# Kernel tuning notes

Hardware: AMD Instinct MI355X
Metric: run time of the kernel (lower is better)

## Reference

```python
import jax, jax.numpy as jnp
import numpy as np
from jax.scipy.special import logsumexp

EPS = 0.05        # entropic regularization (blur^p)
N_ITERS = 20      # Sinkhorn iterations
N, M, D = 8192, 8192, 64


def setup_inputs() -> dict:
    key = jax.random.key(0)
    k1, k2, k3, k4 = jax.random.split(key, 4)
    return {
        "a": jax.random.uniform(k1, (N,), dtype=jnp.float32),
        "x": jax.random.normal(k2, (N, D), dtype=jnp.float32),
        "b": jax.random.uniform(k3, (M,), dtype=jnp.float32),
        "y": jax.random.normal(k4, (M, D), dtype=jnp.float32),
    }


def reference(a, x, b, y):
    eps = EPS
    # _normalize_weights: probability simplex
    a = a / jnp.sum(a)
    b = b / jnp.sum(b)
    loga = jnp.log(a)
    logb = jnp.log(b)
    # squared-Euclidean cost C_ij = ||x_i - y_j||^2, built via one GEMM (online kernel's math)
    x2 = jnp.sum(x * x, axis=1)            # [N]
    y2 = jnp.sum(y * y, axis=1)            # [M]
    C = x2[:, None] + y2[None, :] - 2.0 * (x @ y.T)   # [N, M]

    # log-domain Sinkhorn: f_i = -eps * LSE_j( log b_j + (g_j - C_ij)/eps )
    def softmin_rows(g_, C_, logw):   # reduce over columns j -> [N]
        return -eps * logsumexp(logw[None, :] + (g_[None, :] - C_) / eps, axis=1)

    def softmin_cols(f_, C_, logw):   # reduce over rows i -> [M]
        return -eps * logsumexp(logw[:, None] + (f_[:, None] - C_) / eps, axis=0)

    def body(i, fg):
        f_, g_ = fg
        f_ = softmin_rows(g_, C, logb)
        g_ = softmin_cols(f_, C, loga)
        return (f_, g_)

    f0 = jnp.zeros_like(a)
    g0 = jnp.zeros_like(b)
    f, g = jax.lax.fori_loop(0, N_ITERS, body, (f0, g0))

    # GeomLoss-style: one final symmetric update from detached potentials (Danskin)
    f_d = jax.lax.stop_gradient(f)
    g_d = jax.lax.stop_gradient(g)
    f_fin = softmin_rows(g_d, C, logb)
    g_fin = softmin_cols(f_d, C, loga)
    # OT_eps(a, b) = <a, f> + <b, g>
    return jnp.sum(a * f_fin) + jnp.sum(b * g_fin)
```

## Files before the change

### kernel.cpp

```cpp
#include <hip/hip_runtime.h>
#include <hip/hip_bf16.h>

#define EPS       0.05f
#define N_ITERS   20
#define NR        8192
#define DIM       64
#define LOG2E     1.4426950408889634f
#define LN2       0.6931471805599453f
#define S2        (2.0f * LOG2E / EPS)
#define EPSLN2    (EPS * LN2)
#define NEGINF    (-1e30f)
#define NSPLIT    4

typedef __attribute__((ext_vector_type(8))) short short8;
typedef __attribute__((ext_vector_type(4))) float float4v;

__device__ __forceinline__ float wave_reduce_sum(float v) {
    #pragma unroll
    for (int m = 1; m < 64; m <<= 1) v += __shfl_xor(v, m, 64);
    return v;
}

__device__ __forceinline__ float merge4_l(float2 p0, float2 p1, float2 p2, float2 p3) {
    float M = fmaxf(fmaxf(p0.x, p1.x), fmaxf(p2.x, p3.x));
    float S = p0.y * __builtin_amdgcn_exp2f(p0.x - M)
            + p1.y * __builtin_amdgcn_exp2f(p1.x - M)
            + p2.y * __builtin_amdgcn_exp2f(p2.x - M)
            + p3.y * __builtin_amdgcn_exp2f(p3.x - M);
    return M + __builtin_amdgcn_logf(S);
}

__global__ void sums_kernel(const float* __restrict__ a, const float* __restrict__ b,
                            float* __restrict__ sums) {
    __shared__ float red[32];
    int tid = threadIdx.x;
    float pa = 0.f, pb = 0.f;
    for (int i = tid; i < NR; i += blockDim.x) { pa += a[i]; pb += b[i]; }
    pa = wave_reduce_sum(pa);
    pb = wave_reduce_sum(pb);
    int wid = tid >> 6, ln = tid & 63;
    if (ln == 0) { red[wid] = pa; red[wid + 16] = pb; }
    __syncthreads();
    if (tid == 0) {
        float sa = 0.f, sb = 0.f;
        int nw = blockDim.x >> 6;
        for (int w = 0; w < nw; w++) { sa += red[w]; sb += red[w + 16]; }
        sums[0] = logf(sa); sums[1] = logf(sb); sums[2] = sa; sums[3] = sb;
    }
}

__global__ void prep_kernel(const float* __restrict__ x, const float* __restrict__ y,
                            const float* __restrict__ a, const float* __restrict__ b,
                            const float* __restrict__ sums,
                            short8* __restrict__ xr, short8* __restrict__ yr,
                            short8* __restrict__ xs, short8* __restrict__ ys,
                            float* __restrict__ x2, float* __restrict__ y2,
                            float* __restrict__ la2, float* __restrict__ lb2,
                            float2* __restrict__ Pb) {
    int gid = blockIdx.x * 256 + threadIdx.x;
    bool isx = gid < NR * 8;
    int cid = isx ? gid : gid - NR * 8;
    int row = cid >> 3;
    int c   = cid & 7;
    const float4* src = (const float4*)(isx ? x : y);
    float4 v0 = src[row * 16 + c * 2];
    float4 v1 = src[row * 16 + c * 2 + 1];

    short8 st;
    st[0] = __bfloat16_as_short(__float2bfloat16(v0.x));
    st[1] = __bfloat16_as_short(__float2bfloat16(v0.y));
    st[2] = __bfloat16_as_short(__float2bfloat16(v0.z));
    st[3] = __bfloat16_as_short(__float2bfloat16(v0.w));
    st[4] = __bfloat16_as_short(__float2bfloat16(v1.x));
    st[5] = __bfloat16_as_short(__float2bfloat16(v1.y));
    st[6] = __bfloat16_as_short(__float2bfloat16(v1.z));
    st[7] = __bfloat16_as_short(__float2bfloat16(v1.w));

    (isx ? xr : yr)[row * 8 + c] = st;
    int T = row >> 4, ln = row & 15, f = c >> 2, q = c & 3;
    (isx ? xs : ys)[T * 128 + f * 64 + q * 16 + ln] = st;

    float sq = v0.x*v0.x + v0.y*v0.y + v0.z*v0.z + v0.w*v0.w
             + v1.x*v1.x + v1.y*v1.y + v1.z*v1.z + v1.w*v1.w;
    #pragma unroll
    for (int m = 1; m < 8; m <<= 1) sq += __shfl_xor(sq, m, 64);

    if (c == 0) {
        if (isx) {
            x2[row] = sq;
            la2[row] = (logf(a[row]) - sums[0]) * LOG2E;
        } else {
            y2[row] = sq;
            lb2[row] = (logf(b[row]) - sums[1]) * LOG2E;
            Pb[row] = make_float2(sq * (LOG2E / EPS), 1.0f);
            #pragma unroll
            for (int k = 1; k < NSPLIT; k++)
                Pb[k * NR + row] = make_float2(NEGINF, 0.0f);
        }
    }
}

#define LSE4(acc, c4, mm, ss)                                            \
    {                                                                    \
        float z0 = fmaf(S2, (acc)[0], (c4).x);                           \
        float z1 = fmaf(S2, (acc)[1], (c4).y);                           \
        float z2 = fmaf(S2, (acc)[2], (c4).z);                           \
        float z3 = fmaf(S2, (acc)[3], (c4).w);                           \
        float zm = fmaxf(fmaxf(z0, z1), fmaxf(z2, z3));                  \
        float mn = fmaxf((mm), zm);                                      \
        float e  = __builtin_amdgcn_exp2f((mm) - mn);                    \
        float p  = (__builtin_amdgcn_exp2f(z0 - mn)                      \
                  + __builtin_amdgcn_exp2f(z1 - mn))                     \
                 + (__builtin_amdgcn_exp2f(z2 - mn)                      \
                  + __builtin_amdgcn_exp2f(z3 - mn));                    \
        (ss) = fmaf((ss), e, p);                                         \
        (mm) = mn;                                                       \
    }

__global__ __launch_bounds__(1024, 4) void pass_kernel(
        const short8* __restrict__ matXr,
        const short8* __restrict__ matYs,
        const float2* __restrict__ Pin,
        const float* __restrict__ lw2col,
        float2* __restrict__ Pout) {
    __shared__ __attribute__((aligned(16))) float cbl[2048];
    __shared__ float2 comb[128][9];

    const int tid = threadIdx.x;
    const int bi  = blockIdx.x;
    const int q4  = bi & 3;
    const int rb  = (bi >> 2) * 128;
    const int cb0 = q4 * 2048;

    {
        int j = cb0 + tid * 2;
        float4 p0 = *(const float4*)(Pin + 0 * NR + j);
        float4 p1 = *(const float4*)(Pin + 1 * NR + j);
        float4 p2 = *(const float4*)(Pin + 2 * NR + j);
        float4 p3 = *(const float4*)(Pin + 3 * NR + j);
        float2 lw = *(const float2*)(lw2col + j);
        float2 cb;
        cb.x = lw.x - merge4_l(make_float2(p0.x, p0.y), make_float2(p1.x, p1.y),
                               make_float2(p2.x, p2.y), make_float2(p3.x, p3.y));
        cb.y = lw.y - merge4_l(make_float2(p0.z, p0.w), make_float2(p1.z, p1.w),
                               make_float2(p2.z, p2.w), make_float2(p3.z, p3.w));
        *(float2*)(cbl + tid * 2) = cb;
    }

    const int w     = tid >> 6;
    const int lane  = tid & 63;
    const int quad  = lane >> 4;
    const int ln    = lane & 15;
    const int strip = w & 7;
    const int rh    = w >> 3;

    short8 xf0[4], xf1[4];
    #pragma unroll
    for (int t = 0; t < 4; t++) {
        int r = rb + rh * 64 + t * 16 + ln;
        xf0[t] = matXr[r * 8 + quad];
        xf1[t] = matXr[r * 8 + quad + 4];
    }

    const int T0 = q4 * 128 + strip * 16;
    const short8* yp = matYs + (size_t)T0 * 128 + lane;
    const float* cbs = cbl + strip * 256 + quad * 4;

    float m[4], s[4];
    #pragma unroll
    for (int t = 0; t < 4; t++) { m[t] = NEGINF; s[t] = 0.f; }

    __syncthreads();

    #pragma unroll 2
    for (int jt = 0; jt < 16; jt++) {
        short8 ya0 = yp[0];
        short8 ya1 = yp[64];
        float4 c4  = *(const float4*)(cbs + jt * 16);
        yp += 128;

        float4v acc[4];
        #pragma unroll
        for (int t = 0; t < 4; t++) {
            float4v z = {0.f, 0.f, 0.f, 0.f};
            z = __builtin_amdgcn_mfma_f32_16x16x32_bf16(ya0, xf0[t], z, 0, 0, 0);
            z = __builtin_amdgcn_mfma_f32_16x16x32_bf16(ya1, xf1[t], z, 0, 0, 0);
            acc[t] = z;
        }
        #pragma unroll
        for (int t = 0; t < 4; t++) LSE4(acc[t], c4, m[t], s[t]);
    }

    #pragma unroll
    for (int mask = 16; mask < 64; mask <<= 1) {
        #pragma unroll
        for (int t = 0; t < 4; t++) {
            float mo = __shfl_xor(m[t], mask, 64);
            float so = __shfl_xor(s[t], mask, 64);
            float M  = fmaxf(m[t], mo);
            s[t] = s[t] * __builtin_amdgcn_exp2f(m[t] - M)
                 + so   * __builtin_amdgcn_exp2f(mo   - M);
            m[t] = M;
        }
    }

    if (lane < 16) {
        #pragma unroll
        for (int t = 0; t < 4; t++)
            comb[rh * 64 + t * 16 + ln][strip] = make_float2(m[t], s[t]);
    }
    __syncthreads();

    if (tid < 128) {
        float2 c = comb[tid][0];
        float M = c.x, S = c.y;
        #pragma unroll
        for (int cc = 1; cc < 8; cc++) {
            float2 p = comb[tid][cc];
            float Mn = fmaxf(M, p.x);
            S = S * __builtin_amdgcn_exp2f(M - Mn)
              + p.y * __builtin_amdgcn_exp2f(p.x - Mn);
            M = Mn;
        }
        Pout[q4 * NR + rb + tid] = make_float2(M, S);
    }
}

__global__ void reduce_kernel(const float* __restrict__ a, const float* __restrict__ b,
                              const float* __restrict__ sums,
                              const float* __restrict__ x2, const float* __restrict__ y2,
                              const float2* __restrict__ Pff, const float2* __restrict__ Pgf,
                              float* __restrict__ out) {
    __shared__ float red[32];
    int tid = threadIdx.x;
    float da = 0.f, db = 0.f;
    for (int i = tid; i < NR; i += blockDim.x) {
        float fv = x2[i] - EPSLN2 * merge4_l(Pff[i], Pff[NR + i],
                                             Pff[2 * NR + i], Pff[3 * NR + i]);
        float gv = y2[i] - EPSLN2 * merge4_l(Pgf[i], Pgf[NR + i],
                                             Pgf[2 * NR + i], Pgf[3 * NR + i]);
        da += a[i] * fv;
        db += b[i] * gv;
    }
    da = wave_reduce_sum(da);
    db = wave_reduce_sum(db);
    int wid = tid >> 6, ln = tid & 63;
    if (ln == 0) { red[wid] = da; red[wid + 16] = db; }
    __syncthreads();
    if (tid == 0) {
        float DA = 0.f, DB = 0.f;
        int nw = blockDim.x >> 6;
        for (int w = 0; w < nw; w++) { DA += red[w]; DB += red[w + 16]; }
        out[0] = DA / sums[2] + DB / sums[3];
    }
}

extern "C" void kernel_launch(void* const* d_in, const int* in_sizes, int n_in,
                              void* d_out, int out_size, void* d_ws, size_t ws_size,
                              hipStream_t stream) {
    const float* a = (const float*)d_in[0];
    const float* x = (const float*)d_in[1];
    const float* b = (const float*)d_in[2];
    const float* y = (const float*)d_in[3];

    char* ws = (char*)d_ws;
    short8* xr = (short8*)ws;
    short8* yr = (short8*)(ws + (1 << 20));
    short8* xs = (short8*)(ws + (2 << 20));
    short8* ys = (short8*)(ws + (3 << 20));
    float* fp  = (float*)(ws + (4 << 20));
    float* x2  = fp;
    float* y2  = fp + NR;
    float* la2 = fp + 2 * NR;
    float* lb2 = fp + 3 * NR;
    float2* P   = (float2*)(fp + 4 * NR);
    float2* Pf  = P;
    float2* Pb  = P + NSPLIT * NR;
    float2* Pff = P + 2 * NSPLIT * NR;
    float2* Pgf = P + 3 * NSPLIT * NR;
    float* sums = (float*)(P + 4 * NSPLIT * NR);

    sums_kernel<<<1, 1024, 0, stream>>>(a, b, sums);
    prep_kernel<<<(2 * NR * 8) / 256, 256, 0, stream>>>(x, y, a, b, sums,
                                                        xr, yr, xs, ys,
                                                        x2, y2, la2, lb2, Pb);

    for (int it = 0; it < N_ITERS; it++) {
        pass_kernel<<<256, 1024, 0, stream>>>(xr, ys, Pb, lb2, Pf);
        pass_kernel<<<256, 1024, 0, stream>>>(yr, xs, Pf, la2, Pb);
    }
    pass_kernel<<<256, 1024, 0, stream>>>(xr, ys, Pb, lb2, Pff);
    pass_kernel<<<256, 1024, 0, stream>>>(yr, xs, Pf, la2, Pgf);

    reduce_kernel<<<1, 1024, 0, stream>>>(a, b, sums, x2, y2, Pff, Pgf, (float*)d_out);
}
```

Measured before the change: 944.2 us.

## Stage Y tiles through double-buffered LDS via global_load_lds with staggered start

Instead of each wave streaming its own strip of Y from global memory, the block now cooperatively copies 32KB Y super-tiles into a double-buffered LDS area using direct global-to-LDS loads, and all waves read their fragments from LDS. The starting super-tile is rotated per row block so different blocks hit different parts of Y, which spreads L2 traffic. This adds 64KB of LDS per block and a block-wide barrier per stage, which may reduce occupancy and add sync stalls.

```diff
diff --git a/kernel.cpp b/kernel.cpp
--- a/kernel.cpp
+++ b/kernel.cpp
@@ -123,6 +123,7 @@
         const float2* __restrict__ Pin,
         const float* __restrict__ lw2col,
         float2* __restrict__ Pout) {
+    __shared__ __attribute__((aligned(16))) char ybuf[2][32768];
     __shared__ __attribute__((aligned(16))) float cbl[2048];
     __shared__ float2 comb[128][9];
 
@@ -147,12 +148,12 @@
         *(float2*)(cbl + tid * 2) = cb;
     }
 
-    const int w     = tid >> 6;
-    const int lane  = tid & 63;
-    const int quad  = lane >> 4;
-    const int ln    = lane & 15;
-    const int strip = w & 7;
-    const int rh    = w >> 3;
+    const int w    = tid >> 6;
+    const int lane = tid & 63;
+    const int quad = lane >> 4;
+    const int ln   = lane & 15;
+    const int cs   = w & 7;
+    const int rh   = w >> 3;
 
     short8 xf0[4], xf1[4];
     #pragma unroll
@@ -162,52 +163,80 @@
         xf1[t] = matXr[r * 8 + quad + 4];
     }
 
-    const int T0 = q4 * 128 + strip * 16;
-    const short8* yp = matYs + (size_t)T0 * 128 + lane;
-    const float* cbs = cbl + strip * 256 + quad * 4;
-
-    float m[4], s[4];
-    #pragma unroll
-    for (int t = 0; t < 4; t++) { m[t] = NEGINF; s[t] = 0.f; }
+    const char* ysrc = (const char*)matYs + (size_t)cb0 * 128;
+    const int s0 = (bi >> 2) & 7;
+
+    {
+        const char* src = ysrc + s0 * 32768 + tid * 16;
+        char* dst = &ybuf[0][(tid >> 6) * 1024];
+        __builtin_amdgcn_global_load_lds(
+            (const __attribute__((address_space(1))) void*)src,
+            (__attribute__((address_space(3))) void*)dst, 16, 0, 0);
+        __builtin_amdgcn_global_load_lds(
+            (const __attribute__((address_space(1))) void*)(src + 16384),
+            (__attribute__((address_space(3))) void*)(dst + 16384), 16, 0, 0);
+    }
+
+    float lm[4], ls[4];
+    #pragma unroll
+    for (int t = 0; t < 4; t++) { lm[t] = NEGINF; ls[t] = 0.f; }
 
     __syncthreads();
 
-    #pragma unroll 2
-    for (int jt = 0; jt < 16; jt++) {
-        short8 ya0 = yp[0];
-        short8 ya1 = yp[64];
-        float4 c4  = *(const float4*)(cbs + jt * 16);
-        yp += 128;
-
-        float4v acc[4];
+    for (int t = 0; t < 8; t++) {
+        const int cur = t & 1;
+        const int sc  = (s0 + t) & 7;
+        if (t < 7) {
+            const int sn = (s0 + t + 1) & 7;
+            const char* src = ysrc + sn * 32768 + tid * 16;
+            char* dst = &ybuf[1 - cur][(tid >> 6) * 1024];
+            __builtin_amdgcn_global_load_lds(
+                (const __attribute__((address_space(1))) void*)src,
+                (__attribute__((address_space(3))) void*)dst, 16, 0, 0);
+            __builtin_amdgcn_global_load_lds(
+                (const __attribute__((address_space(1))) void*)(src + 16384),
+                (__attribute__((address_space(3))) void*)(dst + 16384), 16, 0, 0);
+        }
+
+        const char* base = &ybuf[cur][0];
         #pragma unroll
-        for (int t = 0; t < 4; t++) {
-            float4v z = {0.f, 0.f, 0.f, 0.f};
-            z = __builtin_amdgcn_mfma_f32_16x16x32_bf16(ya0, xf0[t], z, 0, 0, 0);
-            z = __builtin_amdgcn_mfma_f32_16x16x32_bf16(ya1, xf1[t], z, 0, 0, 0);
-            acc[t] = z;
-        }
-        #pragma unroll
-        for (int t = 0; t < 4; t++) LSE4(acc[t], c4, m[t], s[t]);
+        for (int uu = 0; uu < 2; uu++) {
+            const int u = 2 * cs + uu;
+            short8 ya0 = *(const short8*)(base + u * 2048 + lane * 16);
+            short8 ya1 = *(const short8*)(base + u * 2048 + 1024 + lane * 16);
+            float4 c4  = *(const float4*)(cbl + sc * 256 + u * 16 + quad * 4);
+
+            float4v acc[4];
+            #pragma unroll
+            for (int tt = 0; tt < 4; tt++) {
+                float4v z = {0.f, 0.f, 0.f, 0.f};
+                z = __builtin_amdgcn_mfma_f32_16x16x32_bf16(ya0, xf0[tt], z, 0, 0, 0);
+                z = __builtin_amdgcn_mfma_f32_16x16x32_bf16(ya1, xf1[tt], z, 0, 0, 0);
+                acc[tt] = z;
+            }
+            #pragma unroll
+            for (int tt = 0; tt < 4; tt++) LSE4(acc[tt], c4, lm[tt], ls[tt]);
+        }
+        __syncthreads();
     }
 
     #pragma unroll
     for (int mask = 16; mask < 64; mask <<= 1) {
         #pragma unroll
         for (int t = 0; t < 4; t++) {
-            float mo = __shfl_xor(m[t], mask, 64);
-            float so = __shfl_xor(s[t], mask, 64);
-            float M  = fmaxf(m[t], mo);
-            s[t] = s[t] * __builtin_amdgcn_exp2f(m[t] - M)
-                 + so   * __builtin_amdgcn_exp2f(mo   - M);
-            m[t] = M;
+            float mo = __shfl_xor(lm[t], mask, 64);
+            float so = __shfl_xor(ls[t], mask, 64);
+            float M  = fmaxf(lm[t], mo);
+            ls[t] = ls[t] * __builtin_amdgcn_exp2f(lm[t] - M)
+                  + so    * __builtin_amdgcn_exp2f(mo    - M);
+            lm[t] = M;
         }
     }
 
     if (lane < 16) {
         #pragma unroll
         for (int t = 0; t < 4; t++)
-            comb[rh * 64 + t * 16 + ln][strip] = make_float2(m[t], s[t]);
+            comb[rh * 64 + t * 16 + ln][cs] = make_float2(lm[t], ls[t]);
     }
     __syncthreads();
 
```

After: 966.8 us. 2.4% more time.
